# Optimization experiments

Measured on AMD Instinct MI355X. Metric: run time of the kernel, lower is better.

The kernel has to match this reference:

```python
import jax, jax.numpy as jnp
import numpy as np

N_NODES = 100000
N_EDGES = 1600000
IN_DIM, HID, OUT = 128, 128, 64


def setup_inputs() -> dict:
    key = jax.random.key(0)
    ks = jax.random.split(key, 8)
    x = jax.random.normal(ks[0], (N_NODES, IN_DIM), dtype=jnp.float32)
    edge_index = jax.random.randint(ks[1], (2, N_EDGES), 0, N_NODES, dtype=jnp.int64)
    # Glorot-ish init for GCNConv linear weights (stored as [in, out]).
    W1 = jax.random.normal(ks[2], (IN_DIM, HID), dtype=jnp.float32) * (1.0 / np.sqrt(IN_DIM))
    b1 = jnp.zeros((HID,), dtype=jnp.float32)
    W2 = jax.random.normal(ks[3], (HID, HID), dtype=jnp.float32) * (1.0 / np.sqrt(HID))
    b2 = jnp.zeros((HID,), dtype=jnp.float32)
    W3 = jax.random.normal(ks[4], (HID, OUT), dtype=jnp.float32) * (1.0 / np.sqrt(HID))
    b3 = jnp.zeros((OUT,), dtype=jnp.float32)
    return {"x": x, "W1": W1, "b1": b1, "W2": W2, "b2": b2,
            "W3": W3, "b3": b3, "edge_index": edge_index}


def _gcn_norm(edge_index, num_nodes):
    # GCNConv default: add self loops, symmetric normalization D^{-1/2} A D^{-1/2}.
    loops = jnp.arange(num_nodes, dtype=edge_index.dtype)
    src = jnp.concatenate([edge_index[0], loops])
    dst = jnp.concatenate([edge_index[1], loops])
    deg = jax.ops.segment_sum(jnp.ones_like(dst, dtype=jnp.float32), dst,
                              num_segments=num_nodes)
    dinv = jnp.where(deg > 0, jax.lax.rsqrt(deg), 0.0)
    norm = dinv[src] * dinv[dst]  # [E + N]
    return src, dst, norm


def _gcn_conv(h, W, b, src, dst, norm, num_nodes):
    h = h @ W                                   # transform first (PyG GCNConv)
    msg = h[src] * norm[:, None]                # gather + scale
    agg = jax.ops.segment_sum(msg, dst, num_segments=num_nodes)  # scatter-add
    return agg + b


def _dropout(h, key, p=0.5):
    keep = jax.random.bernoulli(key, 1.0 - p, h.shape)
    return jnp.where(keep, h / (1.0 - p), 0.0)


def reference(x, W1, b1, W2, b2, W3, b3, edge_index):
    num_nodes = x.shape[0]
    src, dst, norm = _gcn_norm(edge_index, num_nodes)
    kd1, kd2 = jax.random.split(jax.random.key(42))
    h = jax.nn.relu(_gcn_conv(x, W1, b1, src, dst, norm, num_nodes))
    h = _dropout(h, kd1)
    h = jax.nn.relu(_gcn_conv(h, W2, b2, src, dst, norm, num_nodes))
    h = _dropout(h, kd2)
    return _gcn_conv(h, W3, b3, src, dst, norm, num_nodes)
```

## Files before the change

### kernel.cpp

```cpp
#include <hip/hip_runtime.h>
#include <stdint.h>

#define NN 100000
#define NE 1600000
#define NMASKW 400000
#define MASK_BLKS 1563
#define HIST_BLKS 6250
#define WSPL_BLKS 20

typedef float f4 __attribute__((ext_vector_type(4)));
typedef float f2 __attribute__((ext_vector_type(2)));
typedef unsigned short us4 __attribute__((ext_vector_type(4)));
typedef short s16x8 __attribute__((ext_vector_type(8)));

__device__ inline float bf2f(unsigned short u) {
  return __uint_as_float(((uint32_t)u) << 16);
}
__device__ inline unsigned short f2bf(float f) {
  uint32_t u = __float_as_uint(f);
  return (unsigned short)((u + 0x7fffu + ((u >> 16) & 1u)) >> 16);
}
__device__ inline float lo16(uint32_t q) { return __uint_as_float(q << 16); }
__device__ inline float hi16(uint32_t q) { return __uint_as_float(q & 0xffff0000u); }

__host__ __device__ inline void threefry2x32(uint32_t k0, uint32_t k1,
                                             uint32_t x0, uint32_t x1,
                                             uint32_t* y0, uint32_t* y1) {
  uint32_t ks[3] = {k0, k1, k0 ^ k1 ^ 0x1BD11BDAu};
  x0 += ks[0]; x1 += ks[1];
  const uint32_t R[2][4] = {{13u, 15u, 26u, 6u}, {17u, 29u, 16u, 24u}};
#pragma unroll
  for (int i = 0; i < 5; ++i) {
#pragma unroll
    for (int j = 0; j < 4; ++j) {
      uint32_t r = R[i & 1][j];
      x0 += x1;
      x1 = (x1 << r) | (x1 >> (32u - r));
      x1 ^= x0;
    }
    x0 += ks[(i + 1) % 3];
    x1 += ks[(i + 2) % 3] + (uint32_t)(i + 1);
  }
  *y0 = x0; *y1 = x1;
}

__device__ inline uint32_t tf_bits32(uint32_t k0, uint32_t k1, uint32_t idx) {
  uint32_t a, b;
  threefry2x32(k0, k1, 0u, idx, &a, &b);
  return a ^ b;
}

__global__ __launch_bounds__(256) void k_histmask(
    const int* __restrict__ ei, uint32_t* __restrict__ cnt,
    int* __restrict__ slot, uint32_t* __restrict__ m1, uint32_t* __restrict__ m2,
    uint32_t k10, uint32_t k11, uint32_t k20, uint32_t k21) {
  int b = blockIdx.x;
  if (b < MASK_BLKS) {
    int t = b * 256 + threadIdx.x;
    if (t < NMASKW) {
      uint32_t base = (uint32_t)t * 32u;
      uint32_t w1 = 0, w2 = 0;
#pragma unroll 4
      for (int j = 0; j < 32; ++j) {
        w1 |= (tf_bits32(k10, k11, base + j) >> 31) << j;
        w2 |= (tf_bits32(k20, k21, base + j) >> 31) << j;
      }
      m1[t] = w1;
      m2[t] = w2;
    }
  } else {
    int e = (b - MASK_BLKS) * 256 + threadIdx.x;
    if (e < NE) {
      int d = ei[NE + e];
      slot[e] = (int)atomicAdd(&cnt[d], 1u);
    }
  }
}

__global__ __launch_bounds__(256) void k_scan1(const uint32_t* __restrict__ cnt,
                                               uint32_t* __restrict__ rp,
                                               uint32_t* __restrict__ bsum,
                                               float* __restrict__ dinv) {
  __shared__ uint32_t sh[256];
  int t = threadIdx.x;
  int base = blockIdx.x * 1024 + t * 4;
  uint32_t v[4];
  uint32_t s = 0;
#pragma unroll
  for (int i = 0; i < 4; ++i) {
    int idx = base + i;
    v[i] = (idx < NN) ? cnt[idx] : 0u;
    if (idx < NN) dinv[idx] = 1.0f / sqrtf((float)(v[i] + 1u));
    s += v[i];
  }
  sh[t] = s;
  __syncthreads();
  for (int off = 1; off < 256; off <<= 1) {
    uint32_t x = sh[t];
    if (t >= off) x += sh[t - off];
    __syncthreads();
    sh[t] = x;
    __syncthreads();
  }
  uint32_t run = (t > 0) ? sh[t - 1] : 0u;
  if (t == 255) bsum[blockIdx.x] = sh[255];
#pragma unroll
  for (int i = 0; i < 4; ++i) {
    int idx = base + i;
    if (idx < NN) rp[idx] = run;
    run += v[i];
  }
}

__global__ void k_scan2(uint32_t* bsum, int nb) {
  if (threadIdx.x == 0 && blockIdx.x == 0) {
    uint32_t s = 0;
    for (int i = 0; i < nb; ++i) { uint32_t x = bsum[i]; bsum[i] = s; s += x; }
  }
}

__global__ void k_scan3(uint32_t* rp, const uint32_t* __restrict__ bsum) {
  int i = blockIdx.x * 256 + threadIdx.x;
  if (i < NN) rp[i] += bsum[i >> 10];
  if (i == 0) rp[NN] = (uint32_t)NE;
}

__global__ __launch_bounds__(256) void k_scatwsplit(
    const int* __restrict__ ei, const uint32_t* __restrict__ rp,
    const int* __restrict__ slot, int* __restrict__ csrc,
    const float* __restrict__ W1, const float* __restrict__ W2,
    const float* __restrict__ W3,
    unsigned short* __restrict__ w1h, unsigned short* __restrict__ w1l,
    unsigned short* __restrict__ w2h, unsigned short* __restrict__ w2l,
    unsigned short* __restrict__ w3h, unsigned short* __restrict__ w3l) {
  int b = blockIdx.x;
  if (b < WSPL_BLKS) {
    int bb = b * 4 + (threadIdx.x >> 6);
    int lane = threadIdx.x & 63;
    const float* W; unsigned short *H, *L; int dout, j0;
    if (bb < 32)      { W = W1; H = w1h; L = w1l; dout = 128; j0 = bb; }
    else if (bb < 64) { W = W2; H = w2h; L = w2l; dout = 128; j0 = bb - 32; }
    else              { W = W3; H = w3h; L = w3l; dout = 64;  j0 = bb - 64; }
    int kk = j0 & 3;
    int ct = j0 >> 2;
    int kbase = kk * 32 + (lane >> 4) * 8;
    int col = ct * 16 + (lane & 15);
    us4 h0, h1, l0, l1;
#pragma unroll
    for (int j = 0; j < 4; ++j) {
      float v = W[(size_t)(kbase + j) * dout + col];
      h0[j] = f2bf(v);
      l0[j] = f2bf(v - bf2f(h0[j]));
      float v2 = W[(size_t)(kbase + 4 + j) * dout + col];
      h1[j] = f2bf(v2);
      l1[j] = f2bf(v2 - bf2f(h1[j]));
    }
    size_t o = ((size_t)j0 * 64 + lane) * 8;
    *(us4*)(H + o) = h0; *(us4*)(H + o + 4) = h1;
    *(us4*)(L + o) = l0; *(us4*)(L + o + 4) = l1;
  } else {
    int e = (b - WSPL_BLKS) * 256 + threadIdx.x;
    if (e < NE) {
      int s = ei[e];
      int d = ei[NE + e];
      csrc[rp[d] + (uint32_t)slot[e]] = s;
    }
  }
}

__global__ __launch_bounds__(256) void k_gemm1(
    const float* __restrict__ A, const unsigned short* __restrict__ Wh,
    const unsigned short* __restrict__ Wl, unsigned short* __restrict__ C) {
  constexpr int NT = 8;
  const int w = threadIdx.x >> 6;
  const int lane = threadIdx.x & 63;
  const int row0 = blockIdx.x * 64 + w * 16;
  int ar = row0 + (lane & 15);
  if (ar >= NN) ar = NN - 1;
  const int aoff = (lane >> 4) * 8;
  s16x8 afh[4], afl[4];
#pragma unroll
  for (int kk = 0; kk < 4; ++kk) {
    f4 v0 = *(const f4*)(A + (size_t)ar * 128 + kk * 32 + aoff);
    f4 v1 = *(const f4*)(A + (size_t)ar * 128 + kk * 32 + aoff + 4);
#pragma unroll
    for (int j = 0; j < 4; ++j) {
      unsigned short h = f2bf(v0[j]);
      afh[kk][j] = (short)h;
      afl[kk][j] = (short)f2bf(v0[j] - bf2f(h));
      unsigned short h2 = f2bf(v1[j]);
      afh[kk][j + 4] = (short)h2;
      afl[kk][j + 4] = (short)f2bf(v1[j] - bf2f(h2));
    }
  }
  f4 acc[NT];
#pragma unroll
  for (int t = 0; t < NT; ++t) acc[t] = (f4){0.f, 0.f, 0.f, 0.f};
#pragma unroll
  for (int ct = 0; ct < NT; ++ct) {
#pragma unroll
    for (int kk = 0; kk < 4; ++kk) {
      size_t bo = ((size_t)(ct * 4 + kk) * 64 + lane) * 8;
      s16x8 bh = *(const s16x8*)(Wh + bo);
      s16x8 bl = *(const s16x8*)(Wl + bo);
      acc[ct] = __builtin_amdgcn_mfma_f32_16x16x32_bf16(afh[kk], bh, acc[ct], 0, 0, 0);
      acc[ct] = __builtin_amdgcn_mfma_f32_16x16x32_bf16(afh[kk], bl, acc[ct], 0, 0, 0);
      acc[ct] = __builtin_amdgcn_mfma_f32_16x16x32_bf16(afl[kk], bh, acc[ct], 0, 0, 0);
    }
  }
  const int rbase = row0 + (lane >> 4) * 4;
  const int cbase = lane & 15;
#pragma unroll
  for (int ct = 0; ct < NT; ++ct) {
#pragma unroll
    for (int r = 0; r < 4; ++r) {
      int gr = rbase + r;
      if (gr < NN) C[(size_t)gr * 128 + ct * 16 + cbase] = f2bf(acc[ct][r]);
    }
  }
}

template <int DOUT>
__global__ __launch_bounds__(256) void k_gemm_mfma(
    const unsigned short* __restrict__ Ah, const unsigned short* __restrict__ Al,
    const unsigned short* __restrict__ Wh, const unsigned short* __restrict__ Wl,
    unsigned short* __restrict__ C) {
  constexpr int NT = DOUT / 16;
  const int w = threadIdx.x >> 6;
  const int lane = threadIdx.x & 63;
  const int row0 = blockIdx.x * 64 + w * 16;
  int ar = row0 + (lane & 15);
  if (ar >= NN) ar = NN - 1;
  const int aoff = (lane >> 4) * 8;
  s16x8 afh[4], afl[4];
#pragma unroll
  for (int kk = 0; kk < 4; ++kk) {
    afh[kk] = *(const s16x8*)(Ah + (size_t)ar * 128 + kk * 32 + aoff);
    afl[kk] = *(const s16x8*)(Al + (size_t)ar * 128 + kk * 32 + aoff);
  }
  f4 acc[NT];
#pragma unroll
  for (int t = 0; t < NT; ++t) acc[t] = (f4){0.f, 0.f, 0.f, 0.f};
#pragma unroll
  for (int ct = 0; ct < NT; ++ct) {
#pragma unroll
    for (int kk = 0; kk < 4; ++kk) {
      size_t bo = ((size_t)(ct * 4 + kk) * 64 + lane) * 8;
      s16x8 bh = *(const s16x8*)(Wh + bo);
      s16x8 bl = *(const s16x8*)(Wl + bo);
      acc[ct] = __builtin_amdgcn_mfma_f32_16x16x32_bf16(afh[kk], bh, acc[ct], 0, 0, 0);
      acc[ct] = __builtin_amdgcn_mfma_f32_16x16x32_bf16(afh[kk], bl, acc[ct], 0, 0, 0);
      acc[ct] = __builtin_amdgcn_mfma_f32_16x16x32_bf16(afl[kk], bh, acc[ct], 0, 0, 0);
    }
  }
  const int rbase = row0 + (lane >> 4) * 4;
  const int cbase = lane & 15;
#pragma unroll
  for (int ct = 0; ct < NT; ++ct) {
#pragma unroll
    for (int r = 0; r < 4; ++r) {
      int gr = rbase + r;
      if (gr < NN) C[(size_t)gr * DOUT + ct * 16 + cbase] = f2bf(acc[ct][r]);
    }
  }
}

__global__ __launch_bounds__(256) void k_agg_mid(
    const unsigned short* __restrict__ hb, const uint32_t* __restrict__ rp,
    const int* __restrict__ csrc, const float* __restrict__ dinv,
    const float* __restrict__ bias, const uint32_t* __restrict__ mask,
    unsigned short* __restrict__ oh, unsigned short* __restrict__ ol) {
  int wid = __builtin_amdgcn_readfirstlane(blockIdx.x * 4 + (threadIdx.x >> 6));
  if (wid >= NN) return;
  const int lane = threadIdx.x & 63;
  const int q = lane >> 4;
  const int fl = lane & 15;
  const uint32_t beg = rp[wid], end = rp[wid + 1];
  const float dv = dinv[wid];
  const float sn = dv * dv;
  const char* hbase = (const char*)hb;
  f2 acc[4];
#pragma unroll
  for (int j = 0; j < 4; ++j) acc[j] = (f2){0.f, 0.f};

#define ACC4(g, wv)                                                        \
  {                                                                        \
    f2 wv2 = {wv, wv};                                                     \
    f2 h0 = {lo16(g.x), hi16(g.x)}; acc[0] += wv2 * h0;                    \
    f2 h1 = {lo16(g.y), hi16(g.y)}; acc[1] += wv2 * h1;                    \
    f2 h2 = {lo16(g.z), hi16(g.z)}; acc[2] += wv2 * h2;                    \
    f2 h3 = {lo16(g.w), hi16(g.w)}; acc[3] += wv2 * h3;                    \
  }

  uint32_t u = beg;
  for (; u + 16 <= end; u += 16) {
    int s0 = csrc[u + q];
    int s1 = csrc[u + 4 + q];
    int s2 = csrc[u + 8 + q];
    int s3 = csrc[u + 12 + q];
    float w0 = dinv[s0] * dv, w1 = dinv[s1] * dv;
    float w2 = dinv[s2] * dv, w3 = dinv[s3] * dv;
    uint4 g0 = *(const uint4*)(hbase + ((size_t)(uint32_t)s0 << 8) + fl * 16);
    uint4 g1 = *(const uint4*)(hbase + ((size_t)(uint32_t)s1 << 8) + fl * 16);
    uint4 g2 = *(const uint4*)(hbase + ((size_t)(uint32_t)s2 << 8) + fl * 16);
    uint4 g3 = *(const uint4*)(hbase + ((size_t)(uint32_t)s3 << 8) + fl * 16);
    ACC4(g0, w0); ACC4(g1, w1); ACC4(g2, w2); ACC4(g3, w3);
  }
  for (; u < end; u += 4) {
    uint32_t idx = u + (uint32_t)q;
    uint32_t cidx = idx < end ? idx : end - 1u;
    int s = csrc[cidx];
    float w = (idx < end) ? dinv[s] * dv : 0.f;
    uint4 g = *(const uint4*)(hbase + ((size_t)(uint32_t)s << 8) + fl * 16);
    ACC4(g, w);
  }
#undef ACC4

#pragma unroll
  for (int j = 0; j < 4; ++j) {
    acc[j][0] += __shfl_xor(acc[j][0], 16);
    acc[j][1] += __shfl_xor(acc[j][1], 16);
    acc[j][0] += __shfl_xor(acc[j][0], 32);
    acc[j][1] += __shfl_xor(acc[j][1], 32);
  }

  uint4 qs = *(const uint4*)(hbase + ((size_t)(uint32_t)wid << 8) + fl * 16);
  f2 snv = {sn, sn};
  f2 h0 = {lo16(qs.x), hi16(qs.x)};
  f2 h1 = {lo16(qs.y), hi16(qs.y)};
  f2 h2 = {lo16(qs.z), hi16(qs.z)};
  f2 h3 = {lo16(qs.w), hi16(qs.w)};
  acc[0] += snv * h0; acc[1] += snv * h1;
  acc[2] += snv * h2; acc[3] += snv * h3;
#pragma unroll
  for (int j = 0; j < 4; ++j) acc[j] += *(const f2*)(bias + fl * 8 + 2 * j);

  uint32_t mw = mask[(uint32_t)wid * 4u + (uint32_t)(fl >> 2)];
  uint32_t bb = (uint32_t)((fl & 3) * 8);
  uint32_t hw[4], lw[4];
#pragma unroll
  for (int j = 0; j < 4; ++j) {
    float a0 = fmaxf(acc[j][0], 0.f);
    float a1 = fmaxf(acc[j][1], 0.f);
    a0 = ((mw >> (bb + 2 * j)) & 1u) ? 0.f : a0 * 2.f;
    a1 = ((mw >> (bb + 2 * j + 1)) & 1u) ? 0.f : a1 * 2.f;
    unsigned short hh0 = f2bf(a0), hh1 = f2bf(a1);
    unsigned short g0 = f2bf(a0 - bf2f(hh0)), g1 = f2bf(a1 - bf2f(hh1));
    hw[j] = (uint32_t)hh0 | ((uint32_t)hh1 << 16);
    lw[j] = (uint32_t)g0 | ((uint32_t)g1 << 16);
  }
  if (q == 0) {
    uint4 v = {hw[0], hw[1], hw[2], hw[3]};
    *(uint4*)(oh + (size_t)(uint32_t)wid * 128 + fl * 8) = v;
  } else if (q == 1) {
    uint4 v = {lw[0], lw[1], lw[2], lw[3]};
    *(uint4*)(ol + (size_t)(uint32_t)wid * 128 + fl * 8) = v;
  }
}

__global__ __launch_bounds__(256) void k_agg_final(
    const unsigned short* __restrict__ hb, const uint32_t* __restrict__ rp,
    const int* __restrict__ csrc, const float* __restrict__ dinv,
    const float* __restrict__ bias, float* __restrict__ out) {
  int wid = __builtin_amdgcn_readfirstlane(blockIdx.x * 4 + (threadIdx.x >> 6));
  if (wid >= NN) return;
  const int lane = threadIdx.x & 63;
  const int q = lane >> 4;
  const int fl = lane & 15;
  const uint32_t beg = rp[wid], end = rp[wid + 1];
  const float dv = dinv[wid];
  const float sn = dv * dv;
  const char* hbase = (const char*)hb;
  f2 acc[2];
  acc[0] = (f2){0.f, 0.f};
  acc[1] = (f2){0.f, 0.f};

#define ACC2(g, wv)                                                        \
  {                                                                        \
    f2 wv2 = {wv, wv};                                                     \
    f2 h0 = {lo16(g.x), hi16(g.x)}; acc[0] += wv2 * h0;                    \
    f2 h1 = {lo16(g.y), hi16(g.y)}; acc[1] += wv2 * h1;                    \
  }

  uint32_t u = beg;
  for (; u + 16 <= end; u += 16) {
    int s0 = csrc[u + q];
    int s1 = csrc[u + 4 + q];
    int s2 = csrc[u + 8 + q];
    int s3 = csrc[u + 12 + q];
    float w0 = dinv[s0] * dv, w1 = dinv[s1] * dv;
    float w2 = dinv[s2] * dv, w3 = dinv[s3] * dv;
    uint2 g0 = *(const uint2*)(hbase + ((size_t)(uint32_t)s0 << 7) + fl * 8);
    uint2 g1 = *(const uint2*)(hbase + ((size_t)(uint32_t)s1 << 7) + fl * 8);
    uint2 g2 = *(const uint2*)(hbase + ((size_t)(uint32_t)s2 << 7) + fl * 8);
    uint2 g3 = *(const uint2*)(hbase + ((size_t)(uint32_t)s3 << 7) + fl * 8);
    ACC2(g0, w0); ACC2(g1, w1); ACC2(g2, w2); ACC2(g3, w3);
  }
  for (; u < end; u += 4) {
    uint32_t idx = u + (uint32_t)q;
    uint32_t cidx = idx < end ? idx : end - 1u;
    int s = csrc[cidx];
    float w = (idx < end) ? dinv[s] * dv : 0.f;
    uint2 g = *(const uint2*)(hbase + ((size_t)(uint32_t)s << 7) + fl * 8);
    ACC2(g, w);
  }
#undef ACC2

#pragma unroll
  for (int j = 0; j < 2; ++j) {
    acc[j][0] += __shfl_xor(acc[j][0], 16);
    acc[j][1] += __shfl_xor(acc[j][1], 16);
    acc[j][0] += __shfl_xor(acc[j][0], 32);
    acc[j][1] += __shfl_xor(acc[j][1], 32);
  }

  uint2 qs = *(const uint2*)(hbase + ((size_t)(uint32_t)wid << 7) + fl * 8);
  f2 snv = {sn, sn};
  f2 h0 = {lo16(qs.x), hi16(qs.x)};
  f2 h1 = {lo16(qs.y), hi16(qs.y)};
  acc[0] += snv * h0;
  acc[1] += snv * h1;
  acc[0] += *(const f2*)(bias + fl * 4);
  acc[1] += *(const f2*)(bias + fl * 4 + 2);
  if (q == 0) {
    f4 v = {acc[0][0], acc[0][1], acc[1][0], acc[1][1]};
    *(f4*)(out + (size_t)(uint32_t)wid * 64 + fl * 4) = v;
  }
}

extern "C" void kernel_launch(void* const* d_in, const int* in_sizes, int n_in,
                              void* d_out, int out_size, void* d_ws, size_t ws_size,
                              hipStream_t stream) {
  (void)in_sizes; (void)n_in; (void)out_size; (void)ws_size;
  const float* x  = (const float*)d_in[0];
  const float* W1 = (const float*)d_in[1];
  const float* b1 = (const float*)d_in[2];
  const float* W2 = (const float*)d_in[3];
  const float* b2 = (const float*)d_in[4];
  const float* W3 = (const float*)d_in[5];
  const float* b3 = (const float*)d_in[6];
  const int* ei   = (const int*)d_in[7];
  float* out = (float*)d_out;

  char* p = (char*)d_ws;
  auto alloc = [&](size_t bytes) -> void* {
    void* r = (void*)p;
    p += (bytes + 255) & ~(size_t)255;
    return r;
  };
  uint32_t* cnt  = (uint32_t*)alloc((size_t)NN * 4);
  float*    dinv = (float*)alloc((size_t)NN * 4);
  uint32_t* rp   = (uint32_t*)alloc((size_t)(NN + 1) * 4);
  uint32_t* bsum = (uint32_t*)alloc(1024);
  int*      slot = (int*)alloc((size_t)NE * 4);
  int*      csrc = (int*)alloc((size_t)NE * 4);
  uint32_t* m1   = (uint32_t*)alloc((size_t)NMASKW * 4);
  uint32_t* m2   = (uint32_t*)alloc((size_t)NMASKW * 4);
  unsigned short* ah = (unsigned short*)alloc((size_t)NN * 128 * 2);
  unsigned short* al = (unsigned short*)alloc((size_t)NN * 128 * 2);
  unsigned short* hb = (unsigned short*)alloc((size_t)NN * 128 * 2);
  unsigned short* w1h = (unsigned short*)alloc(32 * 64 * 8 * 2);
  unsigned short* w1l = (unsigned short*)alloc(32 * 64 * 8 * 2);
  unsigned short* w2h = (unsigned short*)alloc(32 * 64 * 8 * 2);
  unsigned short* w2l = (unsigned short*)alloc(32 * 64 * 8 * 2);
  unsigned short* w3h = (unsigned short*)alloc(16 * 64 * 8 * 2);
  unsigned short* w3l = (unsigned short*)alloc(16 * 64 * 8 * 2);

  uint32_t kd1a, kd1b, kd2a, kd2b;
  threefry2x32(0u, 42u, 0u, 0u, &kd1a, &kd1b);
  threefry2x32(0u, 42u, 0u, 1u, &kd2a, &kd2b);

  const int gbN = (NN + 255) / 256;
  const int gbScan = (NN + 1023) / 1024;
  const int gbGemm = (NN + 63) / 64;
  const int gbAgg = (NN + 3) / 4;

  hipMemsetAsync(cnt, 0, (size_t)NN * 4, stream);
  k_histmask<<<MASK_BLKS + HIST_BLKS, 256, 0, stream>>>(
      ei, cnt, slot, m1, m2, kd1a, kd1b, kd2a, kd2b);
  k_scan1<<<gbScan, 256, 0, stream>>>(cnt, rp, bsum, dinv);
  k_scan2<<<1, 64, 0, stream>>>(bsum, gbScan);
  k_scan3<<<gbN, 256, 0, stream>>>(rp, bsum);
  k_scatwsplit<<<WSPL_BLKS + HIST_BLKS, 256, 0, stream>>>(
      ei, rp, slot, csrc, W1, W2, W3, w1h, w1l, w2h, w2l, w3h, w3l);

  k_gemm1<<<gbGemm, 256, 0, stream>>>(x, w1h, w1l, hb);
  k_agg_mid<<<gbAgg, 256, 0, stream>>>(hb, rp, csrc, dinv, b1, m1, ah, al);
  k_gemm_mfma<128><<<gbGemm, 256, 0, stream>>>(ah, al, w2h, w2l, hb);
  k_agg_mid<<<gbAgg, 256, 0, stream>>>(hb, rp, csrc, dinv, b2, m2, ah, al);
  k_gemm_mfma<64><<<gbGemm, 256, 0, stream>>>(ah, al, w3h, w3l, hb);
  k_agg_final<<<gbAgg, 256, 0, stream>>>(hb, rp, csrc, dinv, b3, out);
}
```

Baseline: 426.5 us.

## Precompute per-edge normalization weights into packed CSR records and split hist/mask kernels

The CSR build now stores each edge as a packed (source, weight) pair. The weight dinv[s]*dinv[d] is computed once at scatter time, so the three aggregation kernels no longer do a dependent random gather of dinv[s] per edge. Edge-array traffic doubles (8 bytes per edge instead of 4), but one irregular load per edge per layer goes away. The fused histogram+dropout-mask kernel is also split into two separate launches.

```diff
diff --git a/kernel.cpp b/kernel.cpp
--- a/kernel.cpp
+++ b/kernel.cpp
@@ -4,7 +4,6 @@
 #define NN 100000
 #define NE 1600000
 #define NMASKW 400000
-#define MASK_BLKS 1563
 #define HIST_BLKS 6250
 #define WSPL_BLKS 20
 
@@ -50,30 +49,29 @@
   return a ^ b;
 }
 
-__global__ __launch_bounds__(256) void k_histmask(
-    const int* __restrict__ ei, uint32_t* __restrict__ cnt,
-    int* __restrict__ slot, uint32_t* __restrict__ m1, uint32_t* __restrict__ m2,
-    uint32_t k10, uint32_t k11, uint32_t k20, uint32_t k21) {
-  int b = blockIdx.x;
-  if (b < MASK_BLKS) {
-    int t = b * 256 + threadIdx.x;
-    if (t < NMASKW) {
-      uint32_t base = (uint32_t)t * 32u;
-      uint32_t w1 = 0, w2 = 0;
+__global__ __launch_bounds__(256) void k_mask(uint32_t* __restrict__ m1,
+                                              uint32_t* __restrict__ m2,
+                                              uint32_t k10, uint32_t k11,
+                                              uint32_t k20, uint32_t k21) {
+  int t = blockIdx.x * 256 + threadIdx.x;
+  if (t >= NMASKW) return;
+  uint32_t base = (uint32_t)t * 32u;
+  uint32_t w1 = 0, w2 = 0;
 #pragma unroll 4
-      for (int j = 0; j < 32; ++j) {
-        w1 |= (tf_bits32(k10, k11, base + j) >> 31) << j;
-        w2 |= (tf_bits32(k20, k21, base + j) >> 31) << j;
-      }
-      m1[t] = w1;
-      m2[t] = w2;
-    }
-  } else {
-    int e = (b - MASK_BLKS) * 256 + threadIdx.x;
-    if (e < NE) {
-      int d = ei[NE + e];
-      slot[e] = (int)atomicAdd(&cnt[d], 1u);
-    }
+  for (int j = 0; j < 32; ++j) {
+    w1 |= (tf_bits32(k10, k11, base + j) >> 31) << j;
+    w2 |= (tf_bits32(k20, k21, base + j) >> 31) << j;
+  }
+  m1[t] = w1;
+  m2[t] = w2;
+}
+
+__global__ void k_hist(const int* __restrict__ ei, uint32_t* __restrict__ cnt,
+                       int* __restrict__ slot) {
+  int e = blockIdx.x * 256 + threadIdx.x;
+  if (e < NE) {
+    int d = ei[NE + e];
+    slot[e] = (int)atomicAdd(&cnt[d], 1u);
   }
 }
 
@@ -127,7 +125,8 @@
 
 __global__ __launch_bounds__(256) void k_scatwsplit(
     const int* __restrict__ ei, const uint32_t* __restrict__ rp,
-    const int* __restrict__ slot, int* __restrict__ csrc,
+    const int* __restrict__ slot, const float* __restrict__ dinv,
+    uint2* __restrict__ e2,
     const float* __restrict__ W1, const float* __restrict__ W2,
     const float* __restrict__ W3,
     unsigned short* __restrict__ w1h, unsigned short* __restrict__ w1l,
@@ -163,7 +162,11 @@
     if (e < NE) {
       int s = ei[e];
       int d = ei[NE + e];
-      csrc[rp[d] + (uint32_t)slot[e]] = s;
+      float w = dinv[s] * dinv[d];
+      uint2 rec;
+      rec.x = (uint32_t)s;
+      rec.y = __float_as_uint(w);
+      e2[rp[d] + (uint32_t)slot[e]] = rec;
     }
   }
 }
@@ -267,7 +270,7 @@
 
 __global__ __launch_bounds__(256) void k_agg_mid(
     const unsigned short* __restrict__ hb, const uint32_t* __restrict__ rp,
-    const int* __restrict__ csrc, const float* __restrict__ dinv,
+    const uint2* __restrict__ e2, const float* __restrict__ dinv,
     const float* __restrict__ bias, const uint32_t* __restrict__ mask,
     unsigned short* __restrict__ oh, unsigned short* __restrict__ ol) {
   int wid = __builtin_amdgcn_readfirstlane(blockIdx.x * 4 + (threadIdx.x >> 6));
@@ -294,24 +297,24 @@
 
   uint32_t u = beg;
   for (; u + 16 <= end; u += 16) {
-    int s0 = csrc[u + q];
-    int s1 = csrc[u + 4 + q];
-    int s2 = csrc[u + 8 + q];
-    int s3 = csrc[u + 12 + q];
-    float w0 = dinv[s0] * dv, w1 = dinv[s1] * dv;
-    float w2 = dinv[s2] * dv, w3 = dinv[s3] * dv;
-    uint4 g0 = *(const uint4*)(hbase + ((size_t)(uint32_t)s0 << 8) + fl * 16);
-    uint4 g1 = *(const uint4*)(hbase + ((size_t)(uint32_t)s1 << 8) + fl * 16);
-    uint4 g2 = *(const uint4*)(hbase + ((size_t)(uint32_t)s2 << 8) + fl * 16);
-    uint4 g3 = *(const uint4*)(hbase + ((size_t)(uint32_t)s3 << 8) + fl * 16);
+    uint2 r0 = e2[u + q];
+    uint2 r1 = e2[u + 4 + q];
+    uint2 r2 = e2[u + 8 + q];
+    uint2 r3 = e2[u + 12 + q];
+    uint4 g0 = *(const uint4*)(hbase + ((size_t)r0.x << 8) + fl * 16);
+    uint4 g1 = *(const uint4*)(hbase + ((size_t)r1.x << 8) + fl * 16);
+    uint4 g2 = *(const uint4*)(hbase + ((size_t)r2.x << 8) + fl * 16);
+    uint4 g3 = *(const uint4*)(hbase + ((size_t)r3.x << 8) + fl * 16);
+    float w0 = __uint_as_float(r0.y), w1 = __uint_as_float(r1.y);
+    float w2 = __uint_as_float(r2.y), w3 = __uint_as_float(r3.y);
     ACC4(g0, w0); ACC4(g1, w1); ACC4(g2, w2); ACC4(g3, w3);
   }
   for (; u < end; u += 4) {
     uint32_t idx = u + (uint32_t)q;
     uint32_t cidx = idx < end ? idx : end - 1u;
-    int s = csrc[cidx];
-    float w = (idx < end) ? dinv[s] * dv : 0.f;
-    uint4 g = *(const uint4*)(hbase + ((size_t)(uint32_t)s << 8) + fl * 16);
+    uint2 r = e2[cidx];
+    float w = (idx < end) ? __uint_as_float(r.y) : 0.f;
+    uint4 g = *(const uint4*)(hbase + ((size_t)r.x << 8) + fl * 16);
     ACC4(g, w);
   }
 #undef ACC4
@@ -360,7 +363,7 @@
 
 __global__ __launch_bounds__(256) void k_agg_final(
     const unsigned short* __restrict__ hb, const uint32_t* __restrict__ rp,
-    const int* __restrict__ csrc, const float* __restrict__ dinv,
+    const uint2* __restrict__ e2, const float* __restrict__ dinv,
     const float* __restrict__ bias, float* __restrict__ out) {
   int wid = __builtin_amdgcn_readfirstlane(blockIdx.x * 4 + (threadIdx.x >> 6));
   if (wid >= NN) return;
@@ -384,24 +387,24 @@
 
   uint32_t u = beg;
   for (; u + 16 <= end; u += 16) {
-    int s0 = csrc[u + q];
-    int s1 = csrc[u + 4 + q];
-    int s2 = csrc[u + 8 + q];
-    int s3 = csrc[u + 12 + q];
-    float w0 = dinv[s0] * dv, w1 = dinv[s1] * dv;
-    float w2 = dinv[s2] * dv, w3 = dinv[s3] * dv;
-    uint2 g0 = *(const uint2*)(hbase + ((size_t)(uint32_t)s0 << 7) + fl * 8);
-    uint2 g1 = *(const uint2*)(hbase + ((size_t)(uint32_t)s1 << 7) + fl * 8);
-    uint2 g2 = *(const uint2*)(hbase + ((size_t)(uint32_t)s2 << 7) + fl * 8);
-    uint2 g3 = *(const uint2*)(hbase + ((size_t)(uint32_t)s3 << 7) + fl * 8);
+    uint2 r0 = e2[u + q];
+    uint2 r1 = e2[u + 4 + q];
+    uint2 r2 = e2[u + 8 + q];
+    uint2 r3 = e2[u + 12 + q];
+    uint2 g0 = *(const uint2*)(hbase + ((size_t)r0.x << 7) + fl * 8);
+    uint2 g1 = *(const uint2*)(hbase + ((size_t)r1.x << 7) + fl * 8);
+    uint2 g2 = *(const uint2*)(hbase + ((size_t)r2.x << 7) + fl * 8);
+    uint2 g3 = *(const uint2*)(hbase + ((size_t)r3.x << 7) + fl * 8);
+    float w0 = __uint_as_float(r0.y), w1 = __uint_as_float(r1.y);
+    float w2 = __uint_as_float(r2.y), w3 = __uint_as_float(r3.y);
     ACC2(g0, w0); ACC2(g1, w1); ACC2(g2, w2); ACC2(g3, w3);
   }
   for (; u < end; u += 4) {
     uint32_t idx = u + (uint32_t)q;
     uint32_t cidx = idx < end ? idx : end - 1u;
-    int s = csrc[cidx];
-    float w = (idx < end) ? dinv[s] * dv : 0.f;
-    uint2 g = *(const uint2*)(hbase + ((size_t)(uint32_t)s << 7) + fl * 8);
+    uint2 r = e2[cidx];
+    float w = (idx < end) ? __uint_as_float(r.y) : 0.f;
+    uint2 g = *(const uint2*)(hbase + ((size_t)r.x << 7) + fl * 8);
     ACC2(g, w);
   }
 #undef ACC2
@@ -453,7 +456,7 @@
   uint32_t* rp   = (uint32_t*)alloc((size_t)(NN + 1) * 4);
   uint32_t* bsum = (uint32_t*)alloc(1024);
   int*      slot = (int*)alloc((size_t)NE * 4);
-  int*      csrc = (int*)alloc((size_t)NE * 4);
+  uint2*    e2   = (uint2*)alloc((size_t)NE * 8);
   uint32_t* m1   = (uint32_t*)alloc((size_t)NMASKW * 4);
   uint32_t* m2   = (uint32_t*)alloc((size_t)NMASKW * 4);
   unsigned short* ah = (unsigned short*)alloc((size_t)NN * 128 * 2);
@@ -474,20 +477,21 @@
   const int gbScan = (NN + 1023) / 1024;
   const int gbGemm = (NN + 63) / 64;
   const int gbAgg = (NN + 3) / 4;
+  const int gbMask = (NMASKW + 255) / 256;
 
   hipMemsetAsync(cnt, 0, (size_t)NN * 4, stream);
-  k_histmask<<<MASK_BLKS + HIST_BLKS, 256, 0, stream>>>(
-      ei, cnt, slot, m1, m2, kd1a, kd1b, kd2a, kd2b);
+  k_hist<<<HIST_BLKS, 256, 0, stream>>>(ei, cnt, slot);
+  k_mask<<<gbMask, 256, 0, stream>>>(m1, m2, kd1a, kd1b, kd2a, kd2b);
   k_scan1<<<gbScan, 256, 0, stream>>>(cnt, rp, bsum, dinv);
   k_scan2<<<1, 64, 0, stream>>>(bsum, gbScan);
   k_scan3<<<gbN, 256, 0, stream>>>(rp, bsum);
   k_scatwsplit<<<WSPL_BLKS + HIST_BLKS, 256, 0, stream>>>(
-      ei, rp, slot, csrc, W1, W2, W3, w1h, w1l, w2h, w2l, w3h, w3l);
+      ei, rp, slot, dinv, e2, W1, W2, W3, w1h, w1l, w2h, w2l, w3h, w3l);
 
   k_gemm1<<<gbGemm, 256, 0, stream>>>(x, w1h, w1l, hb);
-  k_agg_mid<<<gbAgg, 256, 0, stream>>>(hb, rp, csrc, dinv, b1, m1, ah, al);
+  k_agg_mid<<<gbAgg, 256, 0, stream>>>(hb, rp, e2, dinv, b1, m1, ah, al);
   k_gemm_mfma<128><<<gbGemm, 256, 0, stream>>>(ah, al, w2h, w2l, hb);
-  k_agg_mid<<<gbAgg, 256, 0, stream>>>(hb, rp, csrc, dinv, b2, m2, ah, al);
+  k_agg_mid<<<gbAgg, 256, 0, stream>>>(hb, rp, e2, dinv, b2, m2, ah, al);
   k_gemm_mfma<64><<<gbGemm, 256, 0, stream>>>(ah, al, w3h, w3l, hb);
-  k_agg_final<<<gbAgg, 256, 0, stream>>>(hb, rp, csrc, dinv, b3, out);
-}
+  k_agg_final<<<gbAgg, 256, 0, stream>>>(hb, rp, e2, dinv, b3, out);
+}
```

New measurement: 431.7 us. No clear change (+1.2%).
